# Kernel optimization log

Hardware: AMD Instinct MI355X
Metric: run time of the kernel (lower is better)

## Reference

```python
import jax, jax.numpy as jnp
import numpy as np

IMG_SIZE = 500
FM = 31
RATIOS = [1.0, 2.0, 0.5]
SCALES = [128, 256, 512]
PRE_NMS_TOPN = 1000
POST_NMS_TOPN = 256
IOU_THR = 0.8
VARIANCES = np.array([0.1, 0.1, 0.2, 0.2], np.float32)
BATCH = 64
TOTAL_ANCHORS = FM * FM * len(RATIOS) * len(SCALES)  # 8649


def _generate_anchors():
    # mimics bbox_utils.generate_anchors: normalized grid centers + base sizes
    stride = 1.0 / FM
    ctr = (np.arange(FM, dtype=np.float32) / FM) + stride / 2.0
    gy, gx = np.meshgrid(ctr, ctr, indexing="ij")
    base = []
    for scale in SCALES:
        for ratio in RATIOS:
            w = scale * np.sqrt(ratio) / IMG_SIZE
            h = scale / np.sqrt(ratio) / IMG_SIZE
            base.append([-h / 2, -w / 2, h / 2, w / 2])
    base = np.array(base, np.float32)                        # [9, 4]
    ctrs = np.stack([gy, gx, gy, gx], -1).reshape(-1, 1, 4)  # [FM*FM, 1, 4]
    anc = (ctrs + base[None]).reshape(-1, 4)                 # [8649, 4] yxyx
    return np.clip(anc, 0.0, 1.0)


def setup_inputs() -> dict:
    key = jax.random.key(0)
    k1, k2, k3 = jax.random.split(key, 3)
    return {
        "rpn_bbox_deltas": jax.random.normal(k1, (BATCH, TOTAL_ANCHORS, 4), jnp.float32),
        "rpn_probs": jax.random.uniform(k2, (BATCH, TOTAL_ANCHORS), dtype=jnp.float32),
        "gt_labels": jax.random.randint(k3, (BATCH, 10), 0, 21, jnp.int32),
        "anchors": jnp.asarray(_generate_anchors()),
    }


def _delta_to_bbox(anchors, deltas):
    # anchors [A,4] yxyx broadcast against deltas [B,A,4] (ty,tx,th,tw)
    ah = anchors[..., 2] - anchors[..., 0]
    aw = anchors[..., 3] - anchors[..., 1]
    acy = anchors[..., 0] + 0.5 * ah
    acx = anchors[..., 1] + 0.5 * aw
    h = jnp.exp(deltas[..., 2]) * ah
    w = jnp.exp(deltas[..., 3]) * aw
    cy = deltas[..., 0] * ah + acy
    cx = deltas[..., 1] * aw + acx
    return jnp.stack([cy - 0.5 * h, cx - 0.5 * w, cy + 0.5 * h, cx + 0.5 * w], axis=-1)


def _pairwise_iou(b):
    # b [N,4] yxyx -> [N,N]
    area = (b[:, 2] - b[:, 0]) * (b[:, 3] - b[:, 1])
    y1 = jnp.maximum(b[:, None, 0], b[None, :, 0])
    x1 = jnp.maximum(b[:, None, 1], b[None, :, 1])
    y2 = jnp.minimum(b[:, None, 2], b[None, :, 2])
    x2 = jnp.minimum(b[:, None, 3], b[None, :, 3])
    inter = jnp.maximum(y2 - y1, 0.0) * jnp.maximum(x2 - x1, 0.0)
    union = area[:, None] + area[None, :] - inter
    return inter / jnp.maximum(union, 1e-8)


def _nms_single(boxes, scores):
    # boxes [N,4] already sorted by descending score (from top_k);
    # greedy NMS matching single-class tf.image.combined_non_max_suppression
    n = boxes.shape[0]
    iou = _pairwise_iou(boxes)
    idx = jnp.arange(n)

    def body(keep, i):
        sup = keep[i] & (iou[i] > IOU_THR) & (idx > i)
        return keep & ~sup, None

    keep, _ = jax.lax.scan(body, jnp.ones((n,), bool), jnp.arange(n))
    masked = jnp.where(keep, scores, -1.0)  # scores are probs >= 0
    sel_scores, sel_idx = jax.lax.top_k(masked, POST_NMS_TOPN)
    sel_boxes = jnp.clip(boxes[sel_idx], 0.0, 1.0)  # combined NMS clips boxes
    valid = sel_scores >= 0.0
    return (jnp.where(valid[:, None], sel_boxes, 0.0),
            jnp.where(valid, sel_scores, 0.0))


def reference(rpn_bbox_deltas, rpn_probs, gt_labels, anchors):
    deltas = rpn_bbox_deltas * jnp.asarray(VARIANCES)          # [B,A,4]
    rpn_bboxes = _delta_to_bbox(anchors[None], deltas)         # [B,A,4]
    pre_scores, pre_idx = jax.lax.top_k(rpn_probs, PRE_NMS_TOPN)  # [B,1000]
    pre_boxes = jnp.take_along_axis(rpn_bboxes, pre_idx[..., None], axis=1)
    roi_bboxes, roi_scores = jax.vmap(_nms_single)(pre_boxes, pre_scores)
    return roi_bboxes, roi_scores  # [B,256,4], [B,256]
```

## Files before the change

kernel.cpp:

```cpp
#include <hip/hip_runtime.h>
#include <math.h>

#define BATCH 64
#define A_TOTAL 8649
#define PRE 1000
#define POST 256
#define NBINS 4096
#define NW 16

__global__ __launch_bounds__(1024) void k_topk_decode(
    const float* __restrict__ deltas,
    const float* __restrict__ probs,
    const float* __restrict__ anchors,
    float4* __restrict__ tboxes,
    float* __restrict__ tscores)
{
    #pragma clang fp contract(off)
    const int b = blockIdx.x;
    const int t = threadIdx.x;
    __shared__ unsigned int hist[NBINS];
    __shared__ unsigned int exc[NBINS];
    __shared__ unsigned long long cand[2048];
    __shared__ unsigned int gsum[256];
    __shared__ unsigned int s_thr;
    __shared__ unsigned int s_n;

    for (int i = t; i < NBINS; i += 1024) hist[i] = 0u;
    __syncthreads();

    const float* pr = probs + (size_t)b * A_TOTAL;
    for (int i = t; i < A_TOTAL; i += 1024) {
        unsigned int bits = __float_as_uint(pr[i]);
        atomicAdd(&hist[bits >> 18], 1u);
    }
    __syncthreads();

    if (t < 256) {
        unsigned int gs = 0;
        #pragma unroll
        for (int q = 0; q < 16; ++q) gs += hist[t * 16 + q];
        gsum[t] = gs;
    }
    __syncthreads();
    for (int off = 1; off < 256; off <<= 1) {
        unsigned int add = (t < 256 && t + off < 256) ? gsum[t + off] : 0u;
        __syncthreads();
        if (t < 256) gsum[t] += add;
        __syncthreads();
    }
    if (t < 256) {
        unsigned int run = (t == 255) ? 0u : gsum[t + 1];
        for (int q = 15; q >= 0; --q) {
            int bin = t * 16 + q;
            exc[bin] = run;
            run += hist[bin];
        }
    }
    __syncthreads();
    for (int bin = t; bin < NBINS; bin += 1024) {
        unsigned int ge = exc[bin] + hist[bin];
        unsigned int ge1 = (bin == NBINS - 1) ? 0u : (exc[bin + 1] + hist[bin + 1]);
        if (ge >= PRE && ge1 < PRE) { s_thr = (unsigned int)bin; s_n = ge; }
    }
    __syncthreads();
    const unsigned int T = s_thr;
    const int n = (s_n > 2048u) ? 2048 : (int)s_n;
    for (int i = t; i < NBINS; i += 1024) hist[i] = 0u;
    __syncthreads();

    for (int i = t; i < A_TOTAL; i += 1024) {
        unsigned int bits = __float_as_uint(pr[i]);
        unsigned int bin = bits >> 18;
        if (bin >= T) {
            unsigned int p = exc[bin] + atomicAdd(&hist[bin], 1u);
            if (p < 2048u)
                cand[p] = ((unsigned long long)bits << 32) |
                          (unsigned long long)(0xFFFFFFFFu - (unsigned int)i);
        }
    }
    __syncthreads();

    const float4* anc4 = (const float4*)anchors;
    const float4* dl4  = (const float4*)(deltas + (size_t)b * A_TOTAL * 4);
    for (int p = t; p < n; p += 1024) {
        unsigned long long key = cand[p];
        unsigned int bin = (unsigned int)(key >> 50);
        int segs = (int)exc[bin];
        int sege = (bin > 0) ? (int)exc[bin - 1] : n;
        if (sege > 2048) sege = 2048;
        unsigned int rank = (unsigned int)segs;
        for (int q = segs; q < sege; ++q) rank += (cand[q] > key);
        if (rank >= PRE) continue;
        unsigned int idx = 0xFFFFFFFFu - (unsigned int)(key & 0xFFFFFFFFull);
        float sc = __uint_as_float((unsigned int)(key >> 32));
        float4 a = anc4[idx];
        float4 d = dl4[idx];
        float ah  = a.z - a.x;
        float aw  = a.w - a.y;
        float acy = a.x + 0.5f * ah;
        float acx = a.y + 0.5f * aw;
        float ty = d.x * 0.1f, tx = d.y * 0.1f, th = d.z * 0.2f, tw = d.w * 0.2f;
        float h = (float)exp((double)th) * ah;
        float w = (float)exp((double)tw) * aw;
        float cy = ty * ah + acy;
        float cx = tx * aw + acx;
        float4 bx = make_float4(cy - 0.5f * h, cx - 0.5f * w, cy + 0.5f * h, cx + 0.5f * w);
        tboxes[(size_t)b * PRE + rank] = bx;
        tscores[(size_t)b * PRE + rank] = sc;
    }
}

__global__ __launch_bounds__(256) void k_masks(
    const float4* __restrict__ tboxes,
    unsigned long long* __restrict__ masks)
{
    #pragma clang fp contract(off)
    const int b = blockIdx.y;
    __shared__ float4 sbox[PRE];
    __shared__ float sarea[PRE];
    for (int i = threadIdx.x; i < PRE; i += 256) {
        float4 v = tboxes[(size_t)b * PRE + i];
        sbox[i] = v;
        sarea[i] = (v.z - v.x) * (v.w - v.y);
    }
    __syncthreads();

    int f = blockIdx.x * 4 + (threadIdx.x >> 6);
    int I = 0;
    while (f >= 16 - I) { f -= 16 - I; ++I; }
    const int W = I + f;
    const int lane = threadIdx.x & 63;
    const int row = (I << 6) + lane;
    const int rr = (row < PRE) ? row : 0;
    const float4 bi = sbox[rr];
    const float areai = sarea[rr];
    const int Jbase = W << 6;
    const int jmax = (PRE - Jbase < 64) ? (PRE - Jbase) : 64;
    const double C = (double)0.8f + 0x1p-25;
    const bool diag = (I == W);
    unsigned int mlo = 0u, mhi = 0u;
    for (int jj = 0; jj < jmax; ++jj) {
        const int j = Jbase + jj;
        const float4 bj = sbox[j];
        const float aj = sarea[j];
        float y1 = fmaxf(bi.x, bj.x);
        float x1 = fmaxf(bi.y, bj.y);
        float y2 = fminf(bi.z, bj.z);
        float x2 = fminf(bi.w, bj.w);
        float inter = fmaxf(y2 - y1, 0.0f) * fmaxf(x2 - x1, 0.0f);
        float uni = (areai + aj) - inter;
        float u = fmaxf(uni, 1e-8f);
        bool sup = ((double)inter >= C * (double)u);
        if (diag) sup = sup && (lane < jj);
        unsigned int s = sup ? (1u << (jj & 31)) : 0u;
        if (jj < 32) mlo |= s; else mhi |= s;
    }
    if (row < PRE)
        masks[((size_t)b * PRE + (size_t)row) * NW + W] =
            ((unsigned long long)mhi << 32) | (unsigned long long)mlo;
}

__global__ __launch_bounds__(64) void k_nms_out(
    const float4* __restrict__ tboxes,
    const float* __restrict__ tscores,
    const unsigned long long* __restrict__ masks,
    float* __restrict__ out)
{
    #pragma clang fp contract(off)
    const int b = blockIdx.x;
    const int lane = threadIdx.x;
    const unsigned long long* Mb = masks + (size_t)b * PRE * NW;
    const int wword = lane & 15;
    const int wgrp  = lane >> 4;
    __shared__ int sidx[POST];

    unsigned int dlo[NW], dhi[NW];
    #pragma unroll
    for (int W = 0; W < NW; ++W) {
        const int base = W << 6;
        const int nvalid = (PRE - base < 64) ? (PRE - base) : 64;
        const int drow = base + ((lane < nvalid) ? lane : 0);
        unsigned long long dv = Mb[(size_t)drow * NW + W];
        if (lane >= nvalid) dv = 0ull;
        dlo[W] = (unsigned int)dv;
        dhi[W] = (unsigned int)(dv >> 32);
    }

    unsigned long long rm = 0ull;
    int kc = 0;
    bool done = false;
    #pragma unroll
    for (int W = 0; W < NW; ++W) {
        const int base = W << 6;
        unsigned int rlo = (unsigned int)__builtin_amdgcn_readlane((int)(unsigned int)rm, W)
                         | (unsigned int)__builtin_amdgcn_readlane((int)(unsigned int)rm, W + 16)
                         | (unsigned int)__builtin_amdgcn_readlane((int)(unsigned int)rm, W + 32)
                         | (unsigned int)__builtin_amdgcn_readlane((int)(unsigned int)rm, W + 48);
        unsigned int rhi = (unsigned int)__builtin_amdgcn_readlane((int)(unsigned int)(rm >> 32), W)
                         | (unsigned int)__builtin_amdgcn_readlane((int)(unsigned int)(rm >> 32), W + 16)
                         | (unsigned int)__builtin_amdgcn_readlane((int)(unsigned int)(rm >> 32), W + 32)
                         | (unsigned int)__builtin_amdgcn_readlane((int)(unsigned int)(rm >> 32), W + 48);
        unsigned long long rmW = ((unsigned long long)rhi << 32) | (unsigned long long)rlo;
        unsigned long long valid = (PRE - base >= 64) ? ~0ull : ((1ull << (PRE - base)) - 1ull);
        unsigned long long alive = ~rmW & valid;
        unsigned long long keptw = 0ull;
        while (alive) {
            int i = __builtin_amdgcn_readfirstlane(__ffsll(alive) - 1);
            keptw |= (1ull << i);
            if (lane == 0) sidx[kc] = base + i;
            ++kc;
            if (kc == POST) { done = true; break; }
            unsigned int dl = (unsigned int)__builtin_amdgcn_readlane((int)dlo[W], i);
            unsigned int dh = (unsigned int)__builtin_amdgcn_readlane((int)dhi[W], i);
            unsigned long long d = ((unsigned long long)dh << 32) | (unsigned long long)dl;
            alive &= ~(d | (1ull << i));
        }
        if (done) break;
        unsigned long long kw = keptw;
        while (kw) {
            unsigned long long tA = kw;
            if (wgrp > 0) tA &= tA - 1ull;
            if (wgrp > 1) tA &= tA - 1ull;
            if (wgrp > 2) tA &= tA - 1ull;
            const bool vA = (tA != 0ull);
            const int rA = base + (vA ? (__ffsll(tA) - 1) : 0);
            unsigned long long kw2 = kw;
            kw2 &= kw2 - 1ull; kw2 &= kw2 - 1ull; kw2 &= kw2 - 1ull; kw2 &= kw2 - 1ull;
            unsigned long long tB = kw2;
            if (wgrp > 0) tB &= tB - 1ull;
            if (wgrp > 1) tB &= tB - 1ull;
            if (wgrp > 2) tB &= tB - 1ull;
            const bool vB = (tB != 0ull);
            const int rB = base + (vB ? (__ffsll(tB) - 1) : 0);
            kw = kw2;
            kw &= kw - 1ull; kw &= kw - 1ull; kw &= kw - 1ull; kw &= kw - 1ull;
            unsigned long long mA = Mb[(size_t)rA * NW + wword];
            unsigned long long mB = Mb[(size_t)rB * NW + wword];
            if (!vA || wword < (rA >> 6)) mA = 0ull;
            if (!vB || wword < (rB >> 6)) mB = 0ull;
            rm |= mA | mB;
        }
    }
    __syncthreads();

    const float4* bb = tboxes + (size_t)b * PRE;
    const float* ss = tscores + (size_t)b * PRE;
    float4* oB = (float4*)out + (size_t)b * POST;
    float* oS = out + (size_t)BATCH * POST * 4 + (size_t)b * POST;
    for (int t2 = lane; t2 < POST; t2 += 64) {
        float4 v = make_float4(0.f, 0.f, 0.f, 0.f);
        float sc = 0.f;
        if (t2 < kc) {
            int r = sidx[t2];
            float4 bx = bb[r];
            v.x = fminf(fmaxf(bx.x, 0.f), 1.f);
            v.y = fminf(fmaxf(bx.y, 0.f), 1.f);
            v.z = fminf(fmaxf(bx.z, 0.f), 1.f);
            v.w = fminf(fmaxf(bx.w, 0.f), 1.f);
            sc = ss[r];
        }
        oB[t2] = v;
        oS[t2] = sc;
    }
}

extern "C" void kernel_launch(void* const* d_in, const int* in_sizes, int n_in,
                              void* d_out, int out_size, void* d_ws, size_t ws_size,
                              hipStream_t stream) {
    const float* deltas  = (const float*)d_in[0];
    const float* probs   = (const float*)d_in[1];
    const float* anchors = (const float*)d_in[3];
    float* out = (float*)d_out;

    char* ws = (char*)d_ws;
    float4* tboxes = (float4*)ws;
    float* tscores = (float*)(ws + 1024000);
    unsigned long long* masks = (unsigned long long*)(ws + 1280000);

    k_topk_decode<<<dim3(BATCH), dim3(1024), 0, stream>>>(deltas, probs, anchors, tboxes, tscores);
    k_masks<<<dim3(34, BATCH), dim3(256), 0, stream>>>(tboxes, masks);
    k_nms_out<<<dim3(BATCH), dim3(64), 0, stream>>>(tboxes, tscores, masks, out);
}
```

Before: 99.69 us.

## Stage upper-triangle NMS masks in LDS, precompute areas, wave-scan histogram

The serial NMS kernel now uses 256 threads to cooperatively copy the strictly-upper-triangle mask words into shared memory, so the single scanning wave reads suppression rows from LDS instead of global memory. Diagonal words come from registers via readlane. The mask kernel drops its shared-memory staging, reads boxes and precomputed areas (now written by the decode kernel) directly from global, and unrolls the inner loop for full tiles. The histogram prefix sum is replaced by a single-wave shuffle scan with fewer barriers. The cost is about 60KB of LDS and a bulk copy of the triangle before the serial scan, which may be more than the rows the scan actually touches.

```diff
diff --git a/kernel.cpp b/kernel.cpp
--- a/kernel.cpp
+++ b/kernel.cpp
@@ -7,13 +7,15 @@
 #define POST 256
 #define NBINS 4096
 #define NW 16
+#define TRI_WORDS 7680
 
 __global__ __launch_bounds__(1024) void k_topk_decode(
     const float* __restrict__ deltas,
     const float* __restrict__ probs,
     const float* __restrict__ anchors,
     float4* __restrict__ tboxes,
-    float* __restrict__ tscores)
+    float* __restrict__ tscores,
+    float* __restrict__ tareas)
 {
     #pragma clang fp contract(off)
     const int b = blockIdx.x;
@@ -42,12 +44,25 @@
         gsum[t] = gs;
     }
     __syncthreads();
-    for (int off = 1; off < 256; off <<= 1) {
-        unsigned int add = (t < 256 && t + off < 256) ? gsum[t + off] : 0u;
-        __syncthreads();
-        if (t < 256) gsum[t] += add;
-        __syncthreads();
-    }
+    if (t < 64) {
+        const int l = t;
+        unsigned int a  = gsum[4 * l];
+        unsigned int b2 = gsum[4 * l + 1];
+        unsigned int c  = gsum[4 * l + 2];
+        unsigned int d  = gsum[4 * l + 3];
+        unsigned int quad = a + b2 + c + d;
+        unsigned int q = quad;
+        #pragma unroll
+        for (int off = 1; off < 64; off <<= 1) {
+            unsigned int v = __shfl_down(q, off);
+            q += (l + off < 64) ? v : 0u;
+        }
+        gsum[4 * l]     = q;
+        gsum[4 * l + 1] = q - a;
+        gsum[4 * l + 2] = q - a - b2;
+        gsum[4 * l + 3] = q - a - b2 - c;
+    }
+    __syncthreads();
     if (t < 256) {
         unsigned int run = (t == 255) ? 0u : gsum[t + 1];
         for (int q = 15; q >= 0; --q) {
@@ -107,60 +122,73 @@
         float4 bx = make_float4(cy - 0.5f * h, cx - 0.5f * w, cy + 0.5f * h, cx + 0.5f * w);
         tboxes[(size_t)b * PRE + rank] = bx;
         tscores[(size_t)b * PRE + rank] = sc;
+        tareas[(size_t)b * PRE + rank] = (bx.z - bx.x) * (bx.w - bx.y);
     }
 }
 
 __global__ __launch_bounds__(256) void k_masks(
     const float4* __restrict__ tboxes,
+    const float* __restrict__ tareas,
     unsigned long long* __restrict__ masks)
 {
     #pragma clang fp contract(off)
     const int b = blockIdx.y;
-    __shared__ float4 sbox[PRE];
-    __shared__ float sarea[PRE];
-    for (int i = threadIdx.x; i < PRE; i += 256) {
-        float4 v = tboxes[(size_t)b * PRE + i];
-        sbox[i] = v;
-        sarea[i] = (v.z - v.x) * (v.w - v.y);
-    }
-    __syncthreads();
-
     int f = blockIdx.x * 4 + (threadIdx.x >> 6);
+    f = __builtin_amdgcn_readfirstlane(f);
     int I = 0;
     while (f >= 16 - I) { f -= 16 - I; ++I; }
     const int W = I + f;
     const int lane = threadIdx.x & 63;
     const int row = (I << 6) + lane;
     const int rr = (row < PRE) ? row : 0;
-    const float4 bi = sbox[rr];
-    const float areai = sarea[rr];
-    const int Jbase = W << 6;
-    const int jmax = (PRE - Jbase < 64) ? (PRE - Jbase) : 64;
+    const float4 bi = tboxes[(size_t)b * PRE + rr];
+    const float areai = tareas[(size_t)b * PRE + rr];
+    const float4* __restrict__ bjp = tboxes + (size_t)b * PRE + (W << 6);
+    const float*  __restrict__ ajp = tareas + (size_t)b * PRE + (W << 6);
+    const int jmax = (PRE - (W << 6) < 64) ? (PRE - (W << 6)) : 64;
     const double C = (double)0.8f + 0x1p-25;
     const bool diag = (I == W);
     unsigned int mlo = 0u, mhi = 0u;
-    for (int jj = 0; jj < jmax; ++jj) {
-        const int j = Jbase + jj;
-        const float4 bj = sbox[j];
-        const float aj = sarea[j];
-        float y1 = fmaxf(bi.x, bj.x);
-        float x1 = fmaxf(bi.y, bj.y);
-        float y2 = fminf(bi.z, bj.z);
-        float x2 = fminf(bi.w, bj.w);
-        float inter = fmaxf(y2 - y1, 0.0f) * fmaxf(x2 - x1, 0.0f);
-        float uni = (areai + aj) - inter;
-        float u = fmaxf(uni, 1e-8f);
-        bool sup = ((double)inter >= C * (double)u);
-        if (diag) sup = sup && (lane < jj);
-        unsigned int s = sup ? (1u << (jj & 31)) : 0u;
-        if (jj < 32) mlo |= s; else mhi |= s;
-    }
+
+#define IOU_SUP(jj, sup) do { \
+        const float4 bj = bjp[jj]; \
+        const float aj = ajp[jj]; \
+        float y1 = fmaxf(bi.x, bj.x); \
+        float x1 = fmaxf(bi.y, bj.y); \
+        float y2 = fminf(bi.z, bj.z); \
+        float x2 = fminf(bi.w, bj.w); \
+        float inter = fmaxf(y2 - y1, 0.0f) * fmaxf(x2 - x1, 0.0f); \
+        float uni = (areai + aj) - inter;             \
+        float u = fmaxf(uni, 1e-8f); \
+        sup = ((double)inter >= C * (double)u);       \
+        if (diag) sup = sup && (lane < (jj)); \
+    } while (0)
+
+    if (jmax == 64) {
+        #pragma unroll 4
+        for (int jj = 0; jj < 32; ++jj) {
+            bool sup; IOU_SUP(jj, sup);
+            mlo |= sup ? (1u << jj) : 0u;
+        }
+        #pragma unroll 4
+        for (int jj = 32; jj < 64; ++jj) {
+            bool sup; IOU_SUP(jj, sup);
+            mhi |= sup ? (1u << (jj - 32)) : 0u;
+        }
+    } else {
+        for (int jj = 0; jj < jmax; ++jj) {
+            bool sup; IOU_SUP(jj, sup);
+            unsigned int s = sup ? (1u << (jj & 31)) : 0u;
+            if (jj < 32) mlo |= s; else mhi |= s;
+        }
+    }
+#undef IOU_SUP
     if (row < PRE)
         masks[((size_t)b * PRE + (size_t)row) * NW + W] =
             ((unsigned long long)mhi << 32) | (unsigned long long)mlo;
 }
 
-__global__ __launch_bounds__(64) void k_nms_out(
+__global__ __launch_bounds__(256) void k_nms_out(
     const float4* __restrict__ tboxes,
     const float* __restrict__ tscores,
     const unsigned long long* __restrict__ masks,
@@ -168,86 +196,122 @@
 {
     #pragma clang fp contract(off)
     const int b = blockIdx.x;
-    const int lane = threadIdx.x;
+    const int tid = threadIdx.x;
     const unsigned long long* Mb = masks + (size_t)b * PRE * NW;
-    const int wword = lane & 15;
-    const int wgrp  = lane >> 4;
+    __shared__ unsigned long long Ml[TRI_WORDS];
     __shared__ int sidx[POST];
+    __shared__ int s_kc;
 
     unsigned int dlo[NW], dhi[NW];
+    if (tid < 64) {
+        const int lane = tid;
+        #pragma unroll
+        for (int W = 0; W < NW; ++W) {
+            const int base = W << 6;
+            const int nvalid = (PRE - base < 64) ? (PRE - base) : 64;
+            const int drow = base + ((lane < nvalid) ? lane : 0);
+            unsigned long long dv = Mb[(size_t)drow * NW + W];
+            if (lane >= nvalid) dv = 0ull;
+            dlo[W] = (unsigned int)dv;
+            dhi[W] = (unsigned int)(dv >> 32);
+        }
+    }
+
     #pragma unroll
-    for (int W = 0; W < NW; ++W) {
-        const int base = W << 6;
-        const int nvalid = (PRE - base < 64) ? (PRE - base) : 64;
-        const int drow = base + ((lane < nvalid) ? lane : 0);
-        unsigned long long dv = Mb[(size_t)drow * NW + W];
-        if (lane >= nvalid) dv = 0ull;
-        dlo[W] = (unsigned int)dv;
-        dhi[W] = (unsigned int)(dv >> 32);
-    }
-
-    unsigned long long rm = 0ull;
-    int kc = 0;
-    bool done = false;
-    #pragma unroll
-    for (int W = 0; W < NW; ++W) {
-        const int base = W << 6;
-        unsigned int rlo = (unsigned int)__builtin_amdgcn_readlane((int)(unsigned int)rm, W)
-                         | (unsigned int)__builtin_amdgcn_readlane((int)(unsigned int)rm, W + 16)
-                         | (unsigned int)__builtin_amdgcn_readlane((int)(unsigned int)rm, W + 32)
-                         | (unsigned int)__builtin_amdgcn_readlane((int)(unsigned int)rm, W + 48);
-        unsigned int rhi = (unsigned int)__builtin_amdgcn_readlane((int)(unsigned int)(rm >> 32), W)
-                         | (unsigned int)__builtin_amdgcn_readlane((int)(unsigned int)(rm >> 32), W + 16)
-                         | (unsigned int)__builtin_amdgcn_readlane((int)(unsigned int)(rm >> 32), W + 32)
-                         | (unsigned int)__builtin_amdgcn_readlane((int)(unsigned int)(rm >> 32), W + 48);
-        unsigned long long rmW = ((unsigned long long)rhi << 32) | (unsigned long long)rlo;
-        unsigned long long valid = (PRE - base >= 64) ? ~0ull : ((1ull << (PRE - base)) - 1ull);
-        unsigned long long alive = ~rmW & valid;
-        unsigned long long keptw = 0ull;
-        while (alive) {
-            int i = __builtin_amdgcn_readfirstlane(__ffsll(alive) - 1);
-            keptw |= (1ull << i);
-            if (lane == 0) sidx[kc] = base + i;
-            ++kc;
-            if (kc == POST) { done = true; break; }
-            unsigned int dl = (unsigned int)__builtin_amdgcn_readlane((int)dlo[W], i);
-            unsigned int dh = (unsigned int)__builtin_amdgcn_readlane((int)dhi[W], i);
-            unsigned long long d = ((unsigned long long)dh << 32) | (unsigned long long)dl;
-            alive &= ~(d | (1ull << i));
-        }
-        if (done) break;
-        unsigned long long kw = keptw;
-        while (kw) {
-            unsigned long long tA = kw;
-            if (wgrp > 0) tA &= tA - 1ull;
-            if (wgrp > 1) tA &= tA - 1ull;
-            if (wgrp > 2) tA &= tA - 1ull;
-            const bool vA = (tA != 0ull);
-            const int rA = base + (vA ? (__ffsll(tA) - 1) : 0);
-            unsigned long long kw2 = kw;
-            kw2 &= kw2 - 1ull; kw2 &= kw2 - 1ull; kw2 &= kw2 - 1ull; kw2 &= kw2 - 1ull;
-            unsigned long long tB = kw2;
-            if (wgrp > 0) tB &= tB - 1ull;
-            if (wgrp > 1) tB &= tB - 1ull;
-            if (wgrp > 2) tB &= tB - 1ull;
-            const bool vB = (tB != 0ull);
-            const int rB = base + (vB ? (__ffsll(tB) - 1) : 0);
-            kw = kw2;
-            kw &= kw - 1ull; kw &= kw - 1ull; kw &= kw - 1ull; kw &= kw - 1ull;
-            unsigned long long mA = Mb[(size_t)rA * NW + wword];
-            unsigned long long mB = Mb[(size_t)rB * NW + wword];
-            if (!vA || wword < (rA >> 6)) mA = 0ull;
-            if (!vB || wword < (rB >> 6)) mB = 0ull;
-            rm |= mA | mB;
-        }
-    }
-    __syncthreads();
-
+    for (int I = 0; I < 15; ++I) {
+        const int cnt = 15 - I;
+        const int base = 64 * (15 * I - (I * (I - 1)) / 2);
+        const int total = 64 * cnt;
+        for (int idx = tid; idx < total; idx += 256) {
+            const int r = (I << 6) + idx / cnt;
+            const int w = I + 1 + (idx % cnt);
+            Ml[base + idx] = Mb[(size_t)r * NW + w];
+        }
+    }
+    __syncthreads();
+
+    if (tid < 64) {
+        const int lane = tid;
+        const int wword = lane & 15;
+        const int wgrp  = lane >> 4;
+        unsigned long long rm = 0ull;
+        int kc = 0;
+        bool done = false;
+        #pragma unroll
+        for (int W = 0; W < NW; ++W) {
+            const int base = W << 6;
+            unsigned int rlo = (unsigned int)__builtin_amdgcn_readlane((int)(unsigned int)rm, W)
+                             | (unsigned int)__builtin_amdgcn_readlane((int)(unsigned int)rm, W + 16)
+                             | (unsigned int)__builtin_amdgcn_readlane((int)(unsigned int)rm, W + 32)
+                             | (unsigned int)__builtin_amdgcn_readlane((int)(unsigned int)rm, W + 48);
+            unsigned int rhi = (unsigned int)__builtin_amdgcn_readlane((int)(unsigned int)(rm >> 32), W)
+                             | (unsigned int)__builtin_amdgcn_readlane((int)(unsigned int)(rm >> 32), W + 16)
+                             | (unsigned int)__builtin_amdgcn_readlane((int)(unsigned int)(rm >> 32), W + 32)
+                             | (unsigned int)__builtin_amdgcn_readlane((int)(unsigned int)(rm >> 32), W + 48);
+            unsigned long long rmW = ((unsigned long long)rhi << 32) | (unsigned long long)rlo;
+            unsigned long long valid = (PRE - base >= 64) ? ~0ull : ((1ull << (PRE - base)) - 1ull);
+            unsigned long long alive = ~rmW & valid;
+            unsigned long long keptw = 0ull;
+            while (alive) {
+                int i = __builtin_amdgcn_readfirstlane(__ffsll(alive) - 1);
+                keptw |= (1ull << i);
+                if (lane == 0) sidx[kc] = base + i;
+                ++kc;
+                if (kc == POST) { done = true; break; }
+                unsigned int dl = (unsigned int)__builtin_amdgcn_readlane((int)dlo[W], i);
+                unsigned int dh = (unsigned int)__builtin_amdgcn_readlane((int)dhi[W], i);
+                unsigned long long d = ((unsigned long long)dh << 32) | (unsigned long long)dl;
+                alive &= ~(d | (1ull << i));
+            }
+            if (done) break;
+            const int cntW = 15 - W;
+            const int baseW = 64 * (15 * W - (W * (W - 1)) / 2);
+            unsigned long long kw = keptw;
+            while (kw) {
+                unsigned long long tA = kw;
+                if (wgrp > 0) tA &= tA - 1ull;
+                if (wgrp > 1) tA &= tA - 1ull;
+                if (wgrp > 2) tA &= tA - 1ull;
+                const bool vA = (tA != 0ull);
+                const int iA = vA ? (__ffsll(tA) - 1) : 0;
+                unsigned long long kw2 = kw;
+                kw2 &= kw2 - 1ull; kw2 &= kw2 - 1ull; kw2 &= kw2 - 1ull; kw2 &= kw2 - 1ull;
+                unsigned long long tB = kw2;
+                if (wgrp > 0) tB &= tB - 1ull;
+                if (wgrp > 1) tB &= tB - 1ull;
+                if (wgrp > 2) tB &= tB - 1ull;
+                const bool vB = (tB != 0ull);
+                const int iB = vB ? (__ffsll(tB) - 1) : 0;
+                kw = kw2;
+                kw &= kw - 1ull; kw &= kw - 1ull; kw &= kw - 1ull; kw &= kw - 1ull;
+                unsigned long long lA = 0ull, lB = 0ull;
+                if (wword > W) {
+                    lA = Ml[baseW + iA * cntW + (wword - W - 1)];
+                    lB = Ml[baseW + iB * cntW + (wword - W - 1)];
+                }
+                unsigned long long gA =
+                    ((unsigned long long)(unsigned int)__builtin_amdgcn_readlane((int)dhi[W], iA) << 32)
+                  |  (unsigned long long)(unsigned int)__builtin_amdgcn_readlane((int)dlo[W], iA);
+                unsigned long long gB =
+                    ((unsigned long long)(unsigned int)__builtin_amdgcn_readlane((int)dhi[W], iB) << 32)
+                  |  (unsigned long long)(unsigned int)__builtin_amdgcn_readlane((int)dlo[W], iB);
+                unsigned long long mA = (wword > W) ? lA : ((wword == W) ? gA : 0ull);
+                unsigned long long mB = (wword > W) ? lB : ((wword == W) ? gB : 0ull);
+                if (!vA) mA = 0ull;
+                if (!vB) mB = 0ull;
+                rm |= mA | mB;
+            }
+        }
+        if (tid == 0) s_kc = kc;
+    }
+    __syncthreads();
+
+    const int kc = s_kc;
     const float4* bb = tboxes + (size_t)b * PRE;
     const float* ss = tscores + (size_t)b * PRE;
     float4* oB = (float4*)out + (size_t)b * POST;
     float* oS = out + (size_t)BATCH * POST * 4 + (size_t)b * POST;
-    for (int t2 = lane; t2 < POST; t2 += 64) {
+    for (int t2 = tid; t2 < POST; t2 += 256) {
         float4 v = make_float4(0.f, 0.f, 0.f, 0.f);
         float sc = 0.f;
         if (t2 < kc) {
@@ -276,8 +340,10 @@
     float4* tboxes = (float4*)ws;
     float* tscores = (float*)(ws + 1024000);
     unsigned long long* masks = (unsigned long long*)(ws + 1280000);
-
-    k_topk_decode<<<dim3(BATCH), dim3(1024), 0, stream>>>(deltas, probs, anchors, tboxes, tscores);
-    k_masks<<<dim3(34, BATCH), dim3(256), 0, stream>>>(tboxes, masks);
-    k_nms_out<<<dim3(BATCH), dim3(64), 0, stream>>>(tboxes, tscores, masks, out);
+    float* tareas = (float*)(ws + 9472000);
+
+    k_topk_decode<<<dim3(BATCH), dim3(1024), 0, stream>>>(deltas, probs, anchors,
+                                                          tboxes, tscores, tareas);
+    k_masks<<<dim3(34, BATCH), dim3(256), 0, stream>>>(tboxes, tareas, masks);
+    k_nms_out<<<dim3(BATCH), dim3(256), 0, stream>>>(tboxes, tscores, masks, out);
 }
```

Result: no change. 97.88 us (-1.8%).
